# Optimization experiments

Measured on AMD Instinct MI355X. Metric: run time of the kernel, lower is better.

The kernel has to match this reference:

```python
import jax, jax.numpy as jnp
import numpy as np

N_NODES = 50000
N_EDGES = 800000
IN_FEATS = 128
N_HIDDEN = 64
OUT_FEATS = 40
DIM = 8  # pseudo-coordinate dimension
K = 1    # n_kernels


def setup_inputs() -> dict:
    key = jax.random.key(0)
    ks = jax.random.split(key, 12)
    inp = {
        "features": jax.random.normal(ks[0], (N_NODES, IN_FEATS), dtype=jnp.float32),
        "edge_weight": jax.random.normal(ks[1], (N_EDGES, DIM), dtype=jnp.float32),
        "src": jax.random.randint(ks[2], (N_EDGES,), 0, N_NODES),
        "dst": jax.random.randint(ks[3], (N_EDGES,), 0, N_NODES),
        # layer 1 params (fc has no bias in DGL GMMConv; separate additive bias)
        "W1": jax.random.normal(ks[4], (IN_FEATS, K * N_HIDDEN), dtype=jnp.float32) * (1.0 / np.sqrt(IN_FEATS)),
        "b1": jnp.zeros((N_HIDDEN,), dtype=jnp.float32),
        "mu1": jax.random.normal(ks[5], (K, DIM), dtype=jnp.float32) * 0.1,
        "inv_sigma1": jnp.ones((K, DIM), dtype=jnp.float32),
        # layer 2 params
        "W2": jax.random.normal(ks[6], (N_HIDDEN, K * OUT_FEATS), dtype=jnp.float32) * (1.0 / np.sqrt(N_HIDDEN)),
        "b2": jnp.zeros((OUT_FEATS,), dtype=jnp.float32),
        "mu2": jax.random.normal(ks[7], (K, DIM), dtype=jnp.float32) * 0.1,
        "inv_sigma2": jnp.ones((K, DIM), dtype=jnp.float32),
    }
    return inp


def gmm_conv(x, pseudo, src, dst, W, b, mu, inv_sigma, out_feats):
    # x: [N, in], pseudo: [E, DIM], W: [in, K*out]
    h = (x @ W).reshape(-1, K, out_feats)                      # [N, K, out]
    # gaussian mixture weights per edge/kernel: [E, K]
    diff = pseudo[:, None, :] - mu[None, :, :]                 # [E, K, DIM]
    gw = jnp.exp(-0.5 * jnp.sum(diff * diff * (inv_sigma[None] ** 2), axis=-1))
    # gather src feats, weight, sum over kernels: [E, out]
    msg = jnp.einsum("ekf,ek->ef", h[src], gw)
    agg = jax.ops.segment_sum(msg, dst, num_segments=N_NODES)  # [N, out]
    return agg + b


def reference(features, edge_weight, src, dst, W1, b1, mu1, inv_sigma1, W2, b2, mu2, inv_sigma2):
    x = gmm_conv(features, edge_weight, src, dst, W1, b1, mu1, inv_sigma1, N_HIDDEN)
    x = gmm_conv(x, edge_weight, src, dst, W2, b2, mu2, inv_sigma2, OUT_FEATS)
    return jax.nn.log_softmax(x, axis=1)
```

## Files before the change

### kernel.cpp

```cpp
#include <hip/hip_runtime.h>
#include <hip/hip_fp16.h>
#include <math.h>

#define N_NODES 50000
#define N_EDGES 800000
#define IN_FEATS 128
#define N_HIDDEN 64
#define OUT_FEATS 40
#define DIM 8
#define SCAN_NB ((N_NODES + 255) / 256)
#define EDGE_BLOCKS 1024
#define GT_TILES ((N_NODES + 63) / 64)

typedef _Float16 half8 __attribute__((ext_vector_type(8)));
typedef float floatx4 __attribute__((ext_vector_type(4)));

__device__ __forceinline__ int wave_incl_scan(int x, int lane) {
#pragma unroll
    for (int off = 1; off < 64; off <<= 1) {
        int v = __shfl_up(x, off, 64);
        if (lane >= off) x += v;
    }
    return x;
}

__global__ __launch_bounds__(256) void combo_kernel(
    const float* __restrict__ features, const float* __restrict__ W1,
    const int* __restrict__ src, const int* __restrict__ dst,
    const float* __restrict__ ew,
    const float* __restrict__ mu1, const float* __restrict__ is1,
    const float* __restrict__ mu2, const float* __restrict__ is2,
    int* __restrict__ counts, int2* __restrict__ tmp,
    __half* __restrict__ h1)
{
    const int tid = threadIdx.x;
    __shared__ __align__(16) __half XT[64][136];
    __shared__ __align__(16) __half WT[64][136];

    if (blockIdx.x < EDGE_BLOCKS) {
        for (int e = blockIdx.x * 256 + tid; e < N_EDGES; e += EDGE_BLOCKS * 256) {
            atomicAdd(&counts[dst[e]], 1);
            float s1 = 0.f, s2 = 0.f;
#pragma unroll
            for (int d = 0; d < DIM; ++d) {
                float v = ew[e * DIM + d];
                float d1 = v - mu1[d]; float a1 = is1[d];
                float d2 = v - mu2[d]; float a2 = is2[d];
                s1 += d1 * d1 * a1 * a1;
                s2 += d2 * d2 * a2 * a2;
            }
            __half2 g = __floats2half2_rn(expf(-0.5f * s1), expf(-0.5f * s2));
            int2 rec;
            rec.x = src[e];
            rec.y = *reinterpret_cast<int*>(&g);
            tmp[e] = rec;
        }
        return;
    }

    int tile = blockIdx.x - EDGE_BLOCKS;
    int nodeBase = tile * 64;

    for (int i = tid; i < 64 * 32; i += 256) {
        int row = i >> 5, c4 = i & 31;
        int n = nodeBase + row;
        float4 v = make_float4(0.f, 0.f, 0.f, 0.f);
        if (n < N_NODES) v = ((const float4*)features)[(size_t)n * 32 + c4];
        __half2 h01 = __floats2half2_rn(v.x, v.y);
        __half2 h23 = __floats2half2_rn(v.z, v.w);
        uint2 pk;
        pk.x = *reinterpret_cast<unsigned*>(&h01);
        pk.y = *reinterpret_cast<unsigned*>(&h23);
        *reinterpret_cast<uint2*>(&XT[row][c4 * 4]) = pk;
    }
    for (int rep = 0; rep < 32; ++rep) {
        int idx = tid + rep * 256;
        int k = idx >> 6, n = idx & 63;
        WT[n][k] = __float2half(W1[idx]);
    }
    __syncthreads();

    int lane = tid & 63, w = tid >> 6;
    int m = lane & 15, quad = lane >> 4;

    floatx4 acc0 = {0.f,0.f,0.f,0.f}, acc1 = acc0, acc2 = acc0, acc3 = acc0;
#pragma unroll
    for (int kc = 0; kc < 4; ++kc) {
        half8 a = *(const half8*)&XT[w * 16 + m][kc * 32 + quad * 8];
        half8 b0 = *(const half8*)&WT[ 0 + m][kc * 32 + quad * 8];
        half8 b1 = *(const half8*)&WT[16 + m][kc * 32 + quad * 8];
        half8 b2 = *(const half8*)&WT[32 + m][kc * 32 + quad * 8];
        half8 b3 = *(const half8*)&WT[48 + m][kc * 32 + quad * 8];
        acc0 = __builtin_amdgcn_mfma_f32_16x16x32_f16(a, b0, acc0, 0, 0, 0);
        acc1 = __builtin_amdgcn_mfma_f32_16x16x32_f16(a, b1, acc1, 0, 0, 0);
        acc2 = __builtin_amdgcn_mfma_f32_16x16x32_f16(a, b2, acc2, 0, 0, 0);
        acc3 = __builtin_amdgcn_mfma_f32_16x16x32_f16(a, b3, acc3, 0, 0, 0);
    }
    int nodeRow = nodeBase + w * 16 + quad * 4;
#pragma unroll
    for (int r = 0; r < 4; ++r) {
        int n = nodeRow + r;
        if (n < N_NODES) {
            size_t base = (size_t)n * N_HIDDEN + m;
            h1[base +  0] = __float2half(acc0[r]);
            h1[base + 16] = __float2half(acc1[r]);
            h1[base + 32] = __float2half(acc2[r]);
            h1[base + 48] = __float2half(acc3[r]);
        }
    }
}

__global__ __launch_bounds__(256) void scan_kernel(const int* __restrict__ counts,
                                                   int* __restrict__ offsets,
                                                   int* __restrict__ cursor,
                                                   int* __restrict__ partials) {
    const int tid = threadIdx.x, bid = blockIdx.x;
    int i = bid * 256 + tid;
    int lane = tid & 63, wid = tid >> 6;
    int x = (i < N_NODES) ? counts[i] : 0;
    int incl = wave_incl_scan(x, lane);
    __shared__ int wsum[4];
    __shared__ int sExc, sTot;
    if (lane == 63) wsum[wid] = incl;
    __syncthreads();
    int base = 0;
#pragma unroll
    for (int w = 0; w < 4; ++w)
        if (w < wid) base += wsum[w];
    int lexcl = base + incl - x;
    if (tid == 255) sTot = base + incl;
    __syncthreads();
    if (tid == 0) {
        int T = sTot;
        if (bid == 0) {
            __hip_atomic_store(&partials[0], (T << 2) | 2,
                               __ATOMIC_RELAXED, __HIP_MEMORY_SCOPE_AGENT);
            sExc = 0;
        } else {
            __hip_atomic_store(&partials[bid], (T << 2) | 1,
                               __ATOMIC_RELAXED, __HIP_MEMORY_SCOPE_AGENT);
            int sum = 0, pb = bid - 1;
            while (true) {
                int v = __hip_atomic_load(&partials[pb],
                                          __ATOMIC_RELAXED, __HIP_MEMORY_SCOPE_AGENT);
                if (v == 0) continue;
                sum += v >> 2;
                if ((v & 3) == 2) break;
                --pb;
            }
            __hip_atomic_store(&partials[bid], ((sum + T) << 2) | 2,
                               __ATOMIC_RELAXED, __HIP_MEMORY_SCOPE_AGENT);
            sExc = sum;
        }
    }
    __syncthreads();
    int E = sExc;
    if (i < N_NODES) {
        int v = E + lexcl;
        offsets[i] = v;
        cursor[i]  = v;
    }
    if (bid == SCAN_NB - 1 && tid == 0) offsets[N_NODES] = N_EDGES;
}

__global__ void fill_kernel(const int* __restrict__ dst, const int2* __restrict__ tmp,
                            int* __restrict__ cursor, int2* __restrict__ csr) {
    int e = blockIdx.x * blockDim.x + threadIdx.x;
    if (e >= N_EDGES) return;
    int pos = atomicAdd(&cursor[dst[e]], 1);
    csr[pos] = tmp[e];
}

__global__ __launch_bounds__(256) void agg1_gemm2_kernel(const __half* __restrict__ h,
                                                         const int* __restrict__ offsets,
                                                         const int2* __restrict__ csr,
                                                         const float* __restrict__ b,
                                                         const float* __restrict__ W2,
                                                         __half* __restrict__ h2) {
    __shared__ float xs[8][64];
    const unsigned* h32 = (const unsigned*)h;
    const int tid = threadIdx.x;
    const int w = tid >> 6, lane = tid & 63;
    const int hf = lane >> 5, p = lane & 31;
    const int ln = w * 2 + hf;
    const int n = blockIdx.x * 8 + ln;
    int beg = offsets[n], end = offsets[n + 1];

    float ax = 0.f, ay = 0.f;
    int j = beg;
    for (; j + 4 <= end; j += 4) {
        int2 r0 = csr[j + 0], r1 = csr[j + 1], r2 = csr[j + 2], r3 = csr[j + 3];
        unsigned v0 = h32[(size_t)r0.x * 32 + p];
        unsigned v1 = h32[(size_t)r1.x * 32 + p];
        unsigned v2 = h32[(size_t)r2.x * 32 + p];
        unsigned v3 = h32[(size_t)r3.x * 32 + p];
        float g0 = __low2float(*reinterpret_cast<__half2*>(&r0.y));
        float g1 = __low2float(*reinterpret_cast<__half2*>(&r1.y));
        float g2 = __low2float(*reinterpret_cast<__half2*>(&r2.y));
        float g3 = __low2float(*reinterpret_cast<__half2*>(&r3.y));
        float2 f0 = __half22float2(*reinterpret_cast<__half2*>(&v0));
        float2 f1 = __half22float2(*reinterpret_cast<__half2*>(&v1));
        float2 f2 = __half22float2(*reinterpret_cast<__half2*>(&v2));
        float2 f3 = __half22float2(*reinterpret_cast<__half2*>(&v3));
        ax += f0.x * g0; ay += f0.y * g0;
        ax += f1.x * g1; ay += f1.y * g1;
        ax += f2.x * g2; ay += f2.y * g2;
        ax += f3.x * g3; ay += f3.y * g3;
    }
    for (; j < end; ++j) {
        int2 r = csr[j];
        unsigned v = h32[(size_t)r.x * 32 + p];
        float g = __low2float(*reinterpret_cast<__half2*>(&r.y));
        float2 f = __half22float2(*reinterpret_cast<__half2*>(&v));
        ax += f.x * g; ay += f.y * g;
    }
    float2 bb = *(const float2*)&b[2 * p];
    *(float2*)&xs[ln][2 * p] = make_float2(ax + bb.x, ay + bb.y);
    __syncthreads();

    for (int o = tid; o < 8 * OUT_FEATS; o += 256) {
        int node = o / OUT_FEATS, t = o % OUT_FEATS;
        const float* xr = xs[node];
        float acc = 0.f;
#pragma unroll
        for (int k = 0; k < N_HIDDEN; ++k)
            acc += xr[k] * W2[k * OUT_FEATS + t];
        h2[(size_t)(blockIdx.x * 8 + node) * OUT_FEATS + t] = __float2half(acc);
    }
}

__global__ __launch_bounds__(256) void agg2_kernel(const __half* __restrict__ h,
                                                   const int* __restrict__ offsets,
                                                   const int2* __restrict__ csr,
                                                   const float* __restrict__ b,
                                                   float* __restrict__ out) {
    const unsigned* h32 = (const unsigned*)h;
    const int tid = threadIdx.x;
    const int w = tid >> 6, lane = tid & 63;
    const int hf = lane >> 5, p = lane & 31;
    const int n = blockIdx.x * 8 + w * 2 + hf;
    const int pc = (p < 20) ? p : 19;
    int beg = offsets[n], end = offsets[n + 1];

    float ax = 0.f, ay = 0.f;
    int j = beg;
    for (; j + 4 <= end; j += 4) {
        int2 r0 = csr[j + 0], r1 = csr[j + 1], r2 = csr[j + 2], r3 = csr[j + 3];
        unsigned v0 = h32[(size_t)r0.x * 20 + pc];
        unsigned v1 = h32[(size_t)r1.x * 20 + pc];
        unsigned v2 = h32[(size_t)r2.x * 20 + pc];
        unsigned v3 = h32[(size_t)r3.x * 20 + pc];
        float g0 = __high2float(*reinterpret_cast<__half2*>(&r0.y));
        float g1 = __high2float(*reinterpret_cast<__half2*>(&r1.y));
        float g2 = __high2float(*reinterpret_cast<__half2*>(&r2.y));
        float g3 = __high2float(*reinterpret_cast<__half2*>(&r3.y));
        float2 f0 = __half22float2(*reinterpret_cast<__half2*>(&v0));
        float2 f1 = __half22float2(*reinterpret_cast<__half2*>(&v1));
        float2 f2 = __half22float2(*reinterpret_cast<__half2*>(&v2));
        float2 f3 = __half22float2(*reinterpret_cast<__half2*>(&v3));
        ax += f0.x * g0; ay += f0.y * g0;
        ax += f1.x * g1; ay += f1.y * g1;
        ax += f2.x * g2; ay += f2.y * g2;
        ax += f3.x * g3; ay += f3.y * g3;
    }
    for (; j < end; ++j) {
        int2 r = csr[j];
        unsigned v = h32[(size_t)r.x * 20 + pc];
        float g = __high2float(*reinterpret_cast<__half2*>(&r.y));
        float2 f = __half22float2(*reinterpret_cast<__half2*>(&v));
        ax += f.x * g; ay += f.y * g;
    }

    bool valid = (p < 20);
    float vx = valid ? ax + b[2 * p]     : -INFINITY;
    float vy = valid ? ay + b[2 * p + 1] : -INFINITY;
    float m = fmaxf(vx, vy);
#pragma unroll
    for (int off = 16; off; off >>= 1)
        m = fmaxf(m, __shfl_xor(m, off, 32));
    float ex = valid ? (expf(vx - m) + expf(vy - m)) : 0.f;
#pragma unroll
    for (int off = 16; off; off >>= 1)
        ex += __shfl_xor(ex, off, 32);
    float ls = logf(ex);
    if (valid) {
        float2 o = make_float2(vx - m - ls, vy - m - ls);
        *(float2*)&out[(size_t)n * OUT_FEATS + 2 * p] = o;
    }
}

extern "C" void kernel_launch(void* const* d_in, const int* in_sizes, int n_in,
                              void* d_out, int out_size, void* d_ws, size_t ws_size,
                              hipStream_t stream) {
    const float* features    = (const float*)d_in[0];
    const float* edge_weight = (const float*)d_in[1];
    const int*   src         = (const int*)d_in[2];
    const int*   dst         = (const int*)d_in[3];
    const float* W1          = (const float*)d_in[4];
    const float* b1          = (const float*)d_in[5];
    const float* mu1         = (const float*)d_in[6];
    const float* is1         = (const float*)d_in[7];
    const float* W2          = (const float*)d_in[8];
    const float* b2          = (const float*)d_in[9];
    const float* mu2         = (const float*)d_in[10];
    const float* is2         = (const float*)d_in[11];
    float* out = (float*)d_out;

    int2*   csr     = (int2*)d_ws;
    int2*   tmp     = csr + N_EDGES;
    __half* h1      = (__half*)(tmp + N_EDGES);
    __half* h2      = h1 + (size_t)N_NODES * N_HIDDEN;
    int*    counts  = (int*)(h2 + (size_t)N_NODES * OUT_FEATS);
    int*    partials= counts + N_NODES;
    int*    cursor  = partials + 256;
    int*    offsets = cursor + N_NODES;

    hipMemsetAsync(counts, 0, (N_NODES + 256) * sizeof(int), stream);

    combo_kernel<<<EDGE_BLOCKS + GT_TILES, 256, 0, stream>>>(
        features, W1, src, dst, edge_weight, mu1, is1, mu2, is2, counts, tmp, h1);

    scan_kernel<<<SCAN_NB, 256, 0, stream>>>(counts, offsets, cursor, partials);

    fill_kernel<<<(N_EDGES + 255) / 256, 256, 0, stream>>>(dst, tmp, cursor, csr);

    agg1_gemm2_kernel<<<N_NODES / 8, 256, 0, stream>>>(h1, offsets, csr, b1, W2, h2);

    agg2_kernel<<<N_NODES / 8, 256, 0, stream>>>(h2, offsets, csr, b2, out);
}
```

Baseline: 269.8 us.

## Move layer-1 GEMM from edge kernel into CSR fill kernel

The layer-1 feature GEMM moves out of the combined edge/GEMM kernel and into the CSR fill kernel as extra blocks, while the edge pass becomes a standalone one-edge-per-thread kernel. The GEMM now reads features directly from global memory into registers, with no LDS staging of the feature tile. This rebalances work across launches so the fill's scattered atomics overlap with the dense GEMM. It drops half the shared memory per GEMM block, but the direct global loads may be less coalesced.

```diff
diff --git a/kernel.cpp b/kernel.cpp
--- a/kernel.cpp
+++ b/kernel.cpp
@@ -9,8 +9,8 @@
 #define OUT_FEATS 40
 #define DIM 8
 #define SCAN_NB ((N_NODES + 255) / 256)
-#define EDGE_BLOCKS 1024
 #define GT_TILES ((N_NODES + 63) / 64)
+#define FILL_NB 1024
 
 typedef _Float16 half8 __attribute__((ext_vector_type(8)));
 typedef float floatx4 __attribute__((ext_vector_type(4)));
@@ -24,90 +24,30 @@
     return x;
 }
 
-__global__ __launch_bounds__(256) void combo_kernel(
-    const float* __restrict__ features, const float* __restrict__ W1,
+__global__ __launch_bounds__(256) void edge_kernel(
     const int* __restrict__ src, const int* __restrict__ dst,
     const float* __restrict__ ew,
     const float* __restrict__ mu1, const float* __restrict__ is1,
     const float* __restrict__ mu2, const float* __restrict__ is2,
-    int* __restrict__ counts, int2* __restrict__ tmp,
-    __half* __restrict__ h1)
+    int* __restrict__ counts, int2* __restrict__ tmp)
 {
-    const int tid = threadIdx.x;
-    __shared__ __align__(16) __half XT[64][136];
-    __shared__ __align__(16) __half WT[64][136];
-
-    if (blockIdx.x < EDGE_BLOCKS) {
-        for (int e = blockIdx.x * 256 + tid; e < N_EDGES; e += EDGE_BLOCKS * 256) {
-            atomicAdd(&counts[dst[e]], 1);
-            float s1 = 0.f, s2 = 0.f;
-#pragma unroll
-            for (int d = 0; d < DIM; ++d) {
-                float v = ew[e * DIM + d];
-                float d1 = v - mu1[d]; float a1 = is1[d];
-                float d2 = v - mu2[d]; float a2 = is2[d];
-                s1 += d1 * d1 * a1 * a1;
-                s2 += d2 * d2 * a2 * a2;
-            }
-            __half2 g = __floats2half2_rn(expf(-0.5f * s1), expf(-0.5f * s2));
-            int2 rec;
-            rec.x = src[e];
-            rec.y = *reinterpret_cast<int*>(&g);
-            tmp[e] = rec;
-        }
-        return;
-    }
-
-    int tile = blockIdx.x - EDGE_BLOCKS;
-    int nodeBase = tile * 64;
-
-    for (int i = tid; i < 64 * 32; i += 256) {
-        int row = i >> 5, c4 = i & 31;
-        int n = nodeBase + row;
-        float4 v = make_float4(0.f, 0.f, 0.f, 0.f);
-        if (n < N_NODES) v = ((const float4*)features)[(size_t)n * 32 + c4];
-        __half2 h01 = __floats2half2_rn(v.x, v.y);
-        __half2 h23 = __floats2half2_rn(v.z, v.w);
-        uint2 pk;
-        pk.x = *reinterpret_cast<unsigned*>(&h01);
-        pk.y = *reinterpret_cast<unsigned*>(&h23);
-        *reinterpret_cast<uint2*>(&XT[row][c4 * 4]) = pk;
-    }
-    for (int rep = 0; rep < 32; ++rep) {
-        int idx = tid + rep * 256;
-        int k = idx >> 6, n = idx & 63;
-        WT[n][k] = __float2half(W1[idx]);
-    }
-    __syncthreads();
-
-    int lane = tid & 63, w = tid >> 6;
-    int m = lane & 15, quad = lane >> 4;
-
-    floatx4 acc0 = {0.f,0.f,0.f,0.f}, acc1 = acc0, acc2 = acc0, acc3 = acc0;
-#pragma unroll
-    for (int kc = 0; kc < 4; ++kc) {
-        half8 a = *(const half8*)&XT[w * 16 + m][kc * 32 + quad * 8];
-        half8 b0 = *(const half8*)&WT[ 0 + m][kc * 32 + quad * 8];
-        half8 b1 = *(const half8*)&WT[16 + m][kc * 32 + quad * 8];
-        half8 b2 = *(const half8*)&WT[32 + m][kc * 32 + quad * 8];
-        half8 b3 = *(const half8*)&WT[48 + m][kc * 32 + quad * 8];
-        acc0 = __builtin_amdgcn_mfma_f32_16x16x32_f16(a, b0, acc0, 0, 0, 0);
-        acc1 = __builtin_amdgcn_mfma_f32_16x16x32_f16(a, b1, acc1, 0, 0, 0);
-        acc2 = __builtin_amdgcn_mfma_f32_16x16x32_f16(a, b2, acc2, 0, 0, 0);
-        acc3 = __builtin_amdgcn_mfma_f32_16x16x32_f16(a, b3, acc3, 0, 0, 0);
-    }
-    int nodeRow = nodeBase + w * 16 + quad * 4;
-#pragma unroll
-    for (int r = 0; r < 4; ++r) {
-        int n = nodeRow + r;
-        if (n < N_NODES) {
-            size_t base = (size_t)n * N_HIDDEN + m;
-            h1[base +  0] = __float2half(acc0[r]);
-            h1[base + 16] = __float2half(acc1[r]);
-            h1[base + 32] = __float2half(acc2[r]);
-            h1[base + 48] = __float2half(acc3[r]);
-        }
-    }
+    int e = blockIdx.x * 256 + threadIdx.x;
+    if (e >= N_EDGES) return;
+    atomicAdd(&counts[dst[e]], 1);
+    float s1 = 0.f, s2 = 0.f;
+#pragma unroll
+    for (int d = 0; d < DIM; ++d) {
+        float v = ew[e * DIM + d];
+        float d1 = v - mu1[d]; float a1 = is1[d];
+        float d2 = v - mu2[d]; float a2 = is2[d];
+        s1 += d1 * d1 * a1 * a1;
+        s2 += d2 * d2 * a2 * a2;
+    }
+    __half2 g = __floats2half2_rn(expf(-0.5f * s1), expf(-0.5f * s2));
+    int2 rec;
+    rec.x = src[e];
+    rec.y = *reinterpret_cast<int*>(&g);
+    tmp[e] = rec;
 }
 
 __global__ __launch_bounds__(256) void scan_kernel(const int* __restrict__ counts,
@@ -163,12 +103,69 @@
     if (bid == SCAN_NB - 1 && tid == 0) offsets[N_NODES] = N_EDGES;
 }
 
-__global__ void fill_kernel(const int* __restrict__ dst, const int2* __restrict__ tmp,
-                            int* __restrict__ cursor, int2* __restrict__ csr) {
-    int e = blockIdx.x * blockDim.x + threadIdx.x;
-    if (e >= N_EDGES) return;
-    int pos = atomicAdd(&cursor[dst[e]], 1);
-    csr[pos] = tmp[e];
+__global__ __launch_bounds__(256) void fillgemm_kernel(
+    const float* __restrict__ features, const float* __restrict__ W1,
+    const int* __restrict__ dst, const int2* __restrict__ tmp,
+    int* __restrict__ cursor, int2* __restrict__ csr,
+    __half* __restrict__ h1)
+{
+    const int tid = threadIdx.x;
+    __shared__ __align__(16) __half WT[64][136];
+
+    if (blockIdx.x >= GT_TILES) {
+        int fb = blockIdx.x - GT_TILES;
+        for (int e = fb * 256 + tid; e < N_EDGES; e += FILL_NB * 256) {
+            int pos = atomicAdd(&cursor[dst[e]], 1);
+            csr[pos] = tmp[e];
+        }
+        return;
+    }
+
+    int nodeBase = blockIdx.x * 64;
+    for (int rep = 0; rep < 32; ++rep) {
+        int idx = tid + rep * 256;
+        int k = idx >> 6, n = idx & 63;
+        WT[n][k] = __float2half(W1[idx]);
+    }
+    __syncthreads();
+
+    int lane = tid & 63, w = tid >> 6;
+    int m = lane & 15, quad = lane >> 4;
+    int row = nodeBase + w * 16 + m;
+    int rowc = (row < N_NODES) ? row : (N_NODES - 1);
+    const float* fr = features + (size_t)rowc * IN_FEATS;
+
+    floatx4 acc0 = {0.f,0.f,0.f,0.f}, acc1 = acc0, acc2 = acc0, acc3 = acc0;
+#pragma unroll
+    for (int kc = 0; kc < 4; ++kc) {
+        float4 fa = *(const float4*)(fr + kc * 32 + quad * 8);
+        float4 fb = *(const float4*)(fr + kc * 32 + quad * 8 + 4);
+        union { half8 v; __half2 h2[4]; } A;
+        A.h2[0] = __floats2half2_rn(fa.x, fa.y);
+        A.h2[1] = __floats2half2_rn(fa.z, fa.w);
+        A.h2[2] = __floats2half2_rn(fb.x, fb.y);
+        A.h2[3] = __floats2half2_rn(fb.z, fb.w);
+        half8 b0 = *(const half8*)&WT[ 0 + m][kc * 32 + quad * 8];
+        half8 b1 = *(const half8*)&WT[16 + m][kc * 32 + quad * 8];
+        half8 b2 = *(const half8*)&WT[32 + m][kc * 32 + quad * 8];
+        half8 b3 = *(const half8*)&WT[48 + m][kc * 32 + quad * 8];
+        acc0 = __builtin_amdgcn_mfma_f32_16x16x32_f16(A.v, b0, acc0, 0, 0, 0);
+        acc1 = __builtin_amdgcn_mfma_f32_16x16x32_f16(A.v, b1, acc1, 0, 0, 0);
+        acc2 = __builtin_amdgcn_mfma_f32_16x16x32_f16(A.v, b2, acc2, 0, 0, 0);
+        acc3 = __builtin_amdgcn_mfma_f32_16x16x32_f16(A.v, b3, acc3, 0, 0, 0);
+    }
+    int nodeRow = nodeBase + w * 16 + quad * 4;
+#pragma unroll
+    for (int r = 0; r < 4; ++r) {
+        int n = nodeRow + r;
+        if (n < N_NODES) {
+            size_t base = (size_t)n * N_HIDDEN + m;
+            h1[base +  0] = __float2half(acc0[r]);
+            h1[base + 16] = __float2half(acc1[r]);
+            h1[base + 32] = __float2half(acc2[r]);
+            h1[base + 48] = __float2half(acc3[r]);
+        }
+    }
 }
 
 __global__ __launch_bounds__(256) void agg1_gemm2_kernel(const __half* __restrict__ h,
@@ -317,12 +314,13 @@
 
     hipMemsetAsync(counts, 0, (N_NODES + 256) * sizeof(int), stream);
 
-    combo_kernel<<<EDGE_BLOCKS + GT_TILES, 256, 0, stream>>>(
-        features, W1, src, dst, edge_weight, mu1, is1, mu2, is2, counts, tmp, h1);
+    edge_kernel<<<(N_EDGES + 255) / 256, 256, 0, stream>>>(
+        src, dst, edge_weight, mu1, is1, mu2, is2, counts, tmp);
 
     scan_kernel<<<SCAN_NB, 256, 0, stream>>>(counts, offsets, cursor, partials);
 
-    fill_kernel<<<(N_EDGES + 255) / 256, 256, 0, stream>>>(dst, tmp, cursor, csr);
+    fillgemm_kernel<<<GT_TILES + FILL_NB, 256, 0, stream>>>(
+        features, W1, dst, tmp, cursor, csr, h1);
 
     agg1_gemm2_kernel<<<N_NODES / 8, 256, 0, stream>>>(h1, offsets, csr, b1, W2, h2);
 
```

After: 268.9 us. About the same (-0.3%).
